# Performance work log

Hardware: AMD Instinct MI355X
Metric: run time of the kernel (lower is better)

The kernel has to match this reference:

```python
import jax, jax.numpy as jnp
import numpy as np

B, S, V = 2, 4096, 50265
L, DM, DFF = 2, 768, 3072
H, D, W = 12, 64, 256  # heads, head_dim, one-sided window (attention_window=512)
NEG = -1e9


def _ln(x, s, b, eps=1e-5):
    m = x.mean(-1, keepdims=True)
    v = ((x - m) ** 2).mean(-1, keepdims=True)
    return (x - m) * jax.lax.rsqrt(v + eps) * s + b


def _heads(y):  # [B,S,DM] -> [B,H,S,D]
    return y.reshape(B, S, H, D).transpose(0, 2, 1, 3)


def _longformer_layer(x, am, p):
    nb = S // W  # number of query blocks
    scale = 1.0 / jnp.sqrt(jnp.asarray(D, x.dtype))
    q = _heads(x @ p['Wq'] + p['bq']) * scale
    k = _heads(x @ p['Wk'] + p['bk'])
    v = _heads(x @ p['Wv'] + p['bv'])
    # overlapping key blocks: block n covers padded positions [n*W, n*W+3W)
    idx = jnp.arange(nb)[:, None] * W + jnp.arange(3 * W)[None, :]  # [nb,3W]
    kp = jnp.pad(k, ((0, 0), (0, 0), (W, W), (0, 0)))
    vp = jnp.pad(v, ((0, 0), (0, 0), (W, W), (0, 0)))
    kb = kp[:, :, idx]  # [B,H,nb,3W,D]
    vb = vp[:, :, idx]
    qb = q.reshape(B, H, nb, W, D)
    scores = jnp.einsum('bhnqd,bhnkd->bhnqk', qb, kb)  # [B,H,nb,W,3W]
    # band mask: query i attends keys within +-W
    qi = jnp.arange(W)[:, None]
    kj = jnp.arange(3 * W)[None, :]
    band = (kj >= qi) & (kj <= qi + 2 * W)  # [W,3W]
    kpos = idx - W  # global key positions, [nb,3W]
    valid = (kpos >= 0) & (kpos < S) & (kpos != 0)  # exclude global tok 0 from band
    amk = jnp.pad(am, ((0, 0), (W, W)))[:, idx] > 0  # [B,nb,3W]
    mask = band[None, None, None] & valid[None, None, :, None, :] & amk[:, None, :, None, :]
    scores = jnp.where(mask, scores, NEG).reshape(B, H, S, 3 * W)
    # global-key column: every query attends token 0 (regular K/V)
    sg = jnp.einsum('bhsd,bhd->bhs', q, k[:, :, 0])
    sg = jnp.where(am[:, None, 0:1] > 0, sg, NEG)
    attn = jax.nn.softmax(jnp.concatenate([scores, sg[..., None]], -1), axis=-1)
    a_band = attn[..., :3 * W].reshape(B, H, nb, W, 3 * W)
    out = jnp.einsum('bhnqk,bhnkd->bhnqd', a_band, vb).reshape(B, H, S, D)
    out = out + attn[..., 3 * W][..., None] * v[:, :, 0][:, :, None, :]
    # global query row (token 0): full attention with dedicated global projections
    qg = ((x[:, 0] @ p['Wqg'] + p['bqg']).reshape(B, H, D)) * scale
    kg = _heads(x @ p['Wkg'] + p['bkg'])
    vg = _heads(x @ p['Wvg'] + p['bvg'])
    sgl = jnp.einsum('bhd,bhsd->bhs', qg, kg)
    sgl = jnp.where(am[:, None, :] > 0, sgl, NEG)
    og = jnp.einsum('bhs,bhsd->bhd', jax.nn.softmax(sgl, axis=-1), vg)
    out = out.at[:, :, 0, :].set(og)
    attn_out = out.transpose(0, 2, 1, 3).reshape(B, S, DM) @ p['Wo'] + p['bo']
    x = _ln(x + attn_out, p['ln1_s'], p['ln1_b'])
    h = jax.nn.gelu(x @ p['W1'] + p['b1']) @ p['W2'] + p['b2']
    return _ln(x + h, p['ln2_s'], p['ln2_b'])


def setup_inputs() -> dict:
    key = jax.random.key(0)
    ks = iter(jax.random.split(key, 40))
    f = lambda *s: jax.random.normal(next(ks), s, jnp.float32) * 0.02
    inp = {
        'input_ids': jax.random.randint(next(ks), (B, S), 0, V),
        'attention_mask': jnp.ones((B, S), jnp.int32),
        'word_emb': f(V, DM), 'pos_emb': f(S, DM),
        'ln_e_s': jnp.ones((DM,)), 'ln_e_b': jnp.zeros((DM,)),
        'Wq': f(L, DM, DM), 'bq': jnp.zeros((L, DM)),
        'Wk': f(L, DM, DM), 'bk': jnp.zeros((L, DM)),
        'Wv': f(L, DM, DM), 'bv': jnp.zeros((L, DM)),
        'Wqg': f(L, DM, DM), 'bqg': jnp.zeros((L, DM)),
        'Wkg': f(L, DM, DM), 'bkg': jnp.zeros((L, DM)),
        'Wvg': f(L, DM, DM), 'bvg': jnp.zeros((L, DM)),
        'Wo': f(L, DM, DM), 'bo': jnp.zeros((L, DM)),
        'ln1_s': jnp.ones((L, DM)), 'ln1_b': jnp.zeros((L, DM)),
        'W1': f(L, DM, DFF), 'b1': jnp.zeros((L, DFF)),
        'W2': f(L, DFF, DM), 'b2': jnp.zeros((L, DM)),
        'ln2_s': jnp.ones((L, DM)), 'ln2_b': jnp.zeros((L, DM)),
        'Wcls': f(DM, 2), 'bcls': jnp.zeros((2,)),
    }
    return inp


def reference(input_ids, attention_mask, word_emb, pos_emb, ln_e_s, ln_e_b,
              Wq, bq, Wk, bk, Wv, bv, Wqg, bqg, Wkg, bkg, Wvg, bvg, Wo, bo,
              ln1_s, ln1_b, W1, b1, W2, b2, ln2_s, ln2_b, Wcls, bcls):
    x = word_emb[input_ids] + pos_emb[None]
    x = _ln(x, ln_e_s, ln_e_b)
    for l in range(L):
        p = dict(Wq=Wq[l], bq=bq[l], Wk=Wk[l], bk=bk[l], Wv=Wv[l], bv=bv[l],
                 Wqg=Wqg[l], bqg=bqg[l], Wkg=Wkg[l], bkg=bkg[l], Wvg=Wvg[l], bvg=bvg[l],
                 Wo=Wo[l], bo=bo[l], ln1_s=ln1_s[l], ln1_b=ln1_b[l],
                 W1=W1[l], b1=b1[l], W2=W2[l], b2=b2[l], ln2_s=ln2_s[l], ln2_b=ln2_b[l])
        x = _longformer_layer(x, attention_mask, p)
    return x[:, 0] @ Wcls + bcls  # logits [B, num_labels]
```

## Files before the change

kernel.cpp:

```cpp
#include <hip/hip_runtime.h>
#include <hip/hip_bf16.h>

#define B_   2
#define S_   4096
#define DM_  768
#define H_   12
#define D_   64
#define W_   256
#define NB_  16
#define DFF_ 3072
#define L_   2
#define QS_  3840
#define NEG_ (-1.0e9f)
#define GC_  16
#define QB_  64
#define NCH_ 18

typedef long long ll;
typedef unsigned short u16;
typedef unsigned int   u32;

typedef __attribute__((ext_vector_type(8))) short bfrag;
typedef __attribute__((ext_vector_type(4))) float ffrag;
typedef __attribute__((address_space(1))) unsigned gu32;
typedef __attribute__((address_space(3))) unsigned lu32;

__device__ __forceinline__ float b2f(u16 u){ union{u32 i; float f;} x; x.i = ((u32)u)<<16; return x.f; }
__device__ __forceinline__ u16 f2b(float f){
  __hip_bfloat16 h = __float2bfloat16(f);
  union{__hip_bfloat16 h; u16 u;} x; x.h = h; return x.u;
}
__device__ __forceinline__ void unp8(uint4 u, float* f){
  union{u32 i; float v;} a;
  a.i = u.x<<16; f[0]=a.v; a.i = u.x&0xffff0000u; f[1]=a.v;
  a.i = u.y<<16; f[2]=a.v; a.i = u.y&0xffff0000u; f[3]=a.v;
  a.i = u.z<<16; f[4]=a.v; a.i = u.z&0xffff0000u; f[5]=a.v;
  a.i = u.w<<16; f[6]=a.v; a.i = u.w&0xffff0000u; f[7]=a.v;
}
__device__ __forceinline__ void gld16(const void* g, void* l){
  __builtin_amdgcn_global_load_lds((gu32*)g, (lu32*)l, 16, 0, 0);
}
__device__ __forceinline__ float bsum256(float v, float* s4){
  #pragma unroll
  for(int o=32;o>0;o>>=1) v += __shfl_down(v,o,64);
  int w = threadIdx.x>>6;
  __syncthreads();
  if((threadIdx.x&63)==0) s4[w]=v;
  __syncthreads();
  return s4[0]+s4[1]+s4[2]+s4[3];
}
__device__ __forceinline__ float bmax256(float v, float* s4){
  #pragma unroll
  for(int o=32;o>0;o>>=1) v = fmaxf(v,__shfl_down(v,o,64));
  int w = threadIdx.x>>6;
  __syncthreads();
  if((threadIdx.x&63)==0) s4[w]=v;
  __syncthreads();
  return fmaxf(fmaxf(s4[0],s4[1]),fmaxf(s4[2],s4[3]));
}
__device__ __forceinline__ float gelu_f(float x){
  return 0.5f*x*(1.0f+tanhf(0.7978845608028654f*(x+0.044715f*x*x*x)));
}

__global__ void k_detect(const void* les, int* flag){
  unsigned u = *(const unsigned*)les;
  *flag = (u == 0x3F803F80u) ? 1 : 0;
}

__global__ void k_cvt(const void* __restrict__ src, ll soff, float* __restrict__ dst, int n, const int* flag){
  int f = *flag;
  int i = blockIdx.x*256 + threadIdx.x;
  int st = gridDim.x*256;
  if(f){
    const u16* s = (const u16*)src + soff;
    for(; i<n; i+=st) dst[i] = b2f(s[i]);
  } else {
    const float* s = (const float*)src + soff;
    for(; i<n; i+=st) dst[i] = s[i];
  }
}

struct CvtArgs { const void* src[32]; float* dst[32]; int soff[32]; int n[32]; };
__global__ void k_cvts(CvtArgs a, const int* __restrict__ flag){
  int seg = blockIdx.y;
  int i = blockIdx.x*256 + threadIdx.x;
  if(i >= a.n[seg]) return;
  int f = *flag;
  float v = f ? b2f(((const u16*)a.src[seg])[a.soff[seg]+i])
              : ((const float*)a.src[seg])[a.soff[seg]+i];
  a.dst[seg][i] = v;
}

__global__ __launch_bounds__(256) void k_tw(const void* __restrict__ src, ll soff, u16* __restrict__ dst,
    int R, int C, const int* __restrict__ flag){
  __shared__ float tile[32][33];
  int f = *flag;
  int tx = threadIdx.x & 31, ty = threadIdx.x >> 5;
  int c = blockIdx.x*32 + tx;
  #pragma unroll
  for(int i=0;i<4;i++){
    int r = blockIdx.y*32 + ty + i*8;
    float v;
    if(f) v = b2f(((const u16*)src)[soff + (ll)r*C + c]);
    else  v = ((const float*)src)[soff + (ll)r*C + c];
    tile[ty + i*8][tx] = v;
  }
  __syncthreads();
  #pragma unroll
  for(int i=0;i<4;i++){
    int orow = blockIdx.x*32 + ty + i*8;
    int oc   = blockIdx.y*32 + tx;
    dst[(ll)orow*R + oc] = f2b(tile[tx][ty + i*8]);
  }
}

struct TwArgs { const void* src[14]; ll soff[14]; u16* dst[14]; };
__global__ __launch_bounds__(256) void k_tws(TwArgs a, const int* __restrict__ flag){
  __shared__ float tile[32][33];
  int z = blockIdx.z;
  const void* src = a.src[z]; ll soff = a.soff[z]; u16* dst = a.dst[z];
  int f = *flag;
  int tx = threadIdx.x & 31, ty = threadIdx.x >> 5;
  int c = blockIdx.x*32 + tx;
  #pragma unroll
  for(int i=0;i<4;i++){
    int r = blockIdx.y*32 + ty + i*8;
    float v;
    if(f) v = b2f(((const u16*)src)[soff + (ll)r*DM_ + c]);
    else  v = ((const float*)src)[soff + (ll)r*DM_ + c];
    tile[ty + i*8][tx] = v;
  }
  __syncthreads();
  #pragma unroll
  for(int i=0;i<4;i++){
    int orow = blockIdx.x*32 + ty + i*8;
    int oc   = blockIdx.y*32 + tx;
    dst[(ll)orow*DM_ + oc] = f2b(tile[tx][ty + i*8]);
  }
}

__global__ __launch_bounds__(256) void k_embed(const int* __restrict__ ids, const void* __restrict__ wemb,
    const float* __restrict__ pos, const float* __restrict__ es, const float* __restrict__ eb,
    float* __restrict__ x, u16* __restrict__ xb, const int* flag){
  __shared__ float s4[4];
  int tok = blockIdx.x;
  int s = tok & (S_-1);
  int t = threadIdx.x;
  int id = ids[tok];
  int f = *flag;
  float v[3];
  #pragma unroll
  for(int j=0;j<3;j++){
    int i = t + j*256;
    float we = f ? b2f(((const u16*)wemb)[(ll)id*DM_ + i])
                 : ((const float*)wemb)[(ll)id*DM_ + i];
    v[j] = we + pos[s*DM_ + i];
  }
  float mean = bsum256(v[0]+v[1]+v[2], s4) * (1.0f/DM_);
  float d0=v[0]-mean, d1=v[1]-mean, d2=v[2]-mean;
  float var = bsum256(d0*d0+d1*d1+d2*d2, s4) * (1.0f/DM_);
  float r = rsqrtf(var + 1e-5f);
  #pragma unroll
  for(int j=0;j<3;j++){
    int i = t + j*256;
    float o = (v[j]-mean)*r*es[i] + eb[i];
    x[(ll)tok*DM_ + i] = o;
    xb[(ll)tok*DM_ + i] = f2b(o);
  }
}

__global__ __launch_bounds__(256) void k_rln(float* __restrict__ x, const float* __restrict__ add,
    const float* __restrict__ sc, const float* __restrict__ bi, u16* __restrict__ xb){
  __shared__ float s4[4];
  int tok = blockIdx.x;
  int t = threadIdx.x;
  float v[3];
  #pragma unroll
  for(int j=0;j<3;j++){
    int i = t + j*256;
    v[j] = x[(ll)tok*DM_+i] + add[(ll)tok*DM_+i];
  }
  float mean = bsum256(v[0]+v[1]+v[2], s4) * (1.0f/DM_);
  float d0=v[0]-mean, d1=v[1]-mean, d2=v[2]-mean;
  float var = bsum256(d0*d0+d1*d1+d2*d2, s4) * (1.0f/DM_);
  float r = rsqrtf(var + 1e-5f);
  #pragma unroll
  for(int j=0;j<3;j++){
    int i = t + j*256;
    float o = (v[j]-mean)*r*sc[i] + bi[i];
    x[(ll)tok*DM_+i] = o;
    xb[(ll)tok*DM_+i] = f2b(o);
  }
}

template<int MODE>
__global__ __launch_bounds__(256) void k_mm(const u16* __restrict__ A, const u16* __restrict__ Bt,
    const float* __restrict__ bias, void* __restrict__ Cout, int M, int N, int K){
  __shared__ __align__(16) u16 As[128*32];
  __shared__ __align__(16) u16 Bs[128*32];
  int tid = threadIdx.x, wave = tid>>6, lane = tid&63;
  int m0 = blockIdx.y*128, n0 = blockIdx.x*128;
  int wm = (wave>>1)*64, wn = (wave&1)*64;
  ffrag acc[4][4];
  #pragma unroll
  for(int i=0;i<4;i++)
    #pragma unroll
    for(int j=0;j<4;j++) acc[i][j] = (ffrag){0.f,0.f,0.f,0.f};
  int lrow = lane>>2, lseg = (lane&3)*8;
  const u16* Ap0 = A  + (ll)(m0 + wave*32 + lrow)*K + lseg;
  const u16* Bp0 = Bt + (ll)(n0 + wave*32 + lrow)*K + lseg;
  u16* AsW0 = As + (wave*2+0)*512;
  u16* AsW1 = As + (wave*2+1)*512;
  u16* BsW0 = Bs + (wave*2+0)*512;
  u16* BsW1 = Bs + (wave*2+1)*512;
  int lane15 = lane&15, quad = lane>>4;
  const u16* ArA = As + (wm + lane15)*32 + quad*8;
  const u16* BrB = Bs + (wn + lane15)*32 + quad*8;
  for(int k0=0; k0<K; k0+=32){
    __syncthreads();
    gld16(Ap0 + k0,             AsW0);
    gld16(Ap0 + k0 + (ll)16*K,  AsW1);
    gld16(Bp0 + k0,             BsW0);
    gld16(Bp0 + k0 + (ll)16*K,  BsW1);
    __syncthreads();
    bfrag af[4], bf[4];
    #pragma unroll
    for(int i=0;i<4;i++) af[i] = *(const bfrag*)(ArA + i*512);
    #pragma unroll
    for(int i=0;i<4;i++) bf[i] = *(const bfrag*)(BrB + i*512);
    #pragma unroll
    for(int i=0;i<4;i++)
      #pragma unroll
      for(int j=0;j<4;j++)
        acc[i][j] = __builtin_amdgcn_mfma_f32_16x16x32_bf16(af[i], bf[j], acc[i][j], 0, 0, 0);
  }
  #pragma unroll
  for(int mi=0;mi<4;mi++){
    #pragma unroll
    for(int ni=0;ni<4;ni++){
      int col = n0 + wn + ni*16 + lane15;
      float bv = bias[col];
      #pragma unroll
      for(int r=0;r<4;r++){
        int row = m0 + wm + mi*16 + quad*4 + r;
        float c = acc[mi][ni][r] + bv;
        if(MODE==2) c = gelu_f(c);
        if(MODE==1) ((float*)Cout)[(ll)row*N + col] = c;
        else        ((u16*)Cout)[(ll)row*N + col] = f2b(c);
      }
    }
  }
}

__global__ __launch_bounds__(256) void k_qg(const float* __restrict__ x, const u16* __restrict__ Wt,
    const float* __restrict__ bg, float* __restrict__ qg){
  int b = blockIdx.y;
  int nn = blockIdx.x*256 + threadIdx.x;
  __shared__ float xs[DM_];
  int t = threadIdx.x;
  #pragma unroll
  for(int j=0;j<3;j++) xs[t + j*256] = x[(ll)(b*S_)*DM_ + t + j*256];
  __syncthreads();
  const uint4* wr = (const uint4*)(Wt + (ll)nn*DM_);
  float acc = bg[nn];
  #pragma unroll 4
  for(int g=0; g<96; g++){
    float tf[8]; unp8(wr[g], tf);
    #pragma unroll
    for(int e=0;e<8;e++) acc = fmaf(xs[g*8+e], tf[e], acc);
  }
  qg[b*DM_ + nn] = acc;
}

__global__ __launch_bounds__(256) void k_band(const u16* __restrict__ qb, const u16* __restrict__ kb,
    const u16* __restrict__ vb, const int* __restrict__ am, u16* __restrict__ aout){
  int nq = blockIdx.x, h = blockIdx.y, b = blockIdx.z;
  int q0 = nq*QB_;
  int tid = threadIdx.x;
  int wave = tid>>6, lane = tid&63, lane15 = lane&15, quad = lane>>4;
  int wq = wave*16;
  __shared__ __align__(16) u16 Ks[32*72];
  __shared__ __align__(16) u16 Vt[64*40];
  __shared__ __align__(16) u16 Ps[4][16*40];
  __shared__ __align__(16) float cokA[QB_+2*W_];
  __shared__ __align__(16) float k0f[64];
  __shared__ __align__(16) float v0f[64];
  const int kbase = q0 - W_;
  const int am0 = am[b*S_];
  for(int i=tid; i<QB_+2*W_; i+=256){
    int kp = kbase + i;
    cokA[i] = ((kp>=1) && (kp<S_) && (am[b*S_+kp]>0)) ? 0.f : NEG_;
  }
  if(tid < 64){
    k0f[tid] = b2f(kb[(ll)(b*S_)*QS_ + h*64 + tid]);
    v0f[tid] = b2f(vb[(ll)(b*S_)*QS_ + h*64 + tid]);
  }
  bfrag aq[2];
  {
    const u16* qbase = qb + ((ll)(b*S_ + q0 + wq + lane15))*QS_ + h*64 + quad*8;
    aq[0] = *(const bfrag*)(qbase);
    aq[1] = *(const bfrag*)(qbase + 32);
  }
  ffrag ao[4];
  #pragma unroll
  for(int j=0;j<4;j++) ao[j] = (ffrag){0.f,0.f,0.f,0.f};
  float ms = -INFINITY, ls = 0.f;

  int c_lo = (kbase < 1) ? ((1 - kbase) / 32) : 0;
  if(c_lo < 0) c_lo = 0;
  int c_hi = (S_ - 1 - kbase) / 32 + 1;
  if(c_hi > NCH_) c_hi = NCH_;

  int skey = tid>>3, sseg = tid&7;
  uint4 kreg;
  union { u16 s[8]; uint4 v; } vreg;
  auto FETCH = [&](int c){
    int kp0 = kbase + c*32;
    if(kp0 >= 0 && kp0 + 31 < S_){
      kreg = *(const uint4*)(kb + ((ll)(b*S_ + kp0 + skey))*QS_ + h*64 + sseg*8);
      const u16* vp = vb + ((ll)(b*S_ + kp0 + wave*8))*QS_ + h*64 + lane;
      #pragma unroll
      for(int j=0;j<8;j++) vreg.s[j] = vp[(ll)j*QS_];
    } else {
      int kp = kp0 + skey;
      kreg = make_uint4(0,0,0,0);
      if((unsigned)kp < (unsigned)S_)
        kreg = *(const uint4*)(kb + ((ll)(b*S_+kp))*QS_ + h*64 + sseg*8);
      #pragma unroll
      for(int j=0;j<8;j++){
        int kp2 = kp0 + wave*8 + j;
        vreg.s[j] = ((unsigned)kp2 < (unsigned)S_) ? vb[((ll)(b*S_+kp2))*QS_ + h*64 + lane] : (u16)0;
      }
    }
  };
  FETCH(c_lo);

  #pragma unroll 1
  for(int c=c_lo; c<c_hi; c++){
    __syncthreads();
    *(uint4*)&Ks[skey*72 + sseg*8] = kreg;
    *(uint4*)&Vt[lane*40 + wave*8] = vreg.v;
    __syncthreads();
    if(c+1 < c_hi) FETCH(c+1);
    ffrag st0 = (ffrag){0.f,0.f,0.f,0.f};
    ffrag st1 = (ffrag){0.f,0.f,0.f,0.f};
    #pragma unroll
    for(int kc=0;kc<2;kc++){
      bfrag k0r = *(const bfrag*)&Ks[(     lane15)*72 + kc*32 + quad*8];
      bfrag k1r = *(const bfrag*)&Ks[(16 + lane15)*72 + kc*32 + quad*8];
      st0 = __builtin_amdgcn_mfma_f32_16x16x32_bf16(k0r, aq[kc], st0, 0, 0, 0);
      st1 = __builtin_amdgcn_mfma_f32_16x16x32_bf16(k1r, aq[kc], st1, 0, 0, 0);
    }
    float4 ck0 = *(const float4*)&cokA[c*32 + quad*4];
    float4 ck1 = *(const float4*)&cokA[c*32 + 16 + quad*4];
    float cka[8] = {ck0.x,ck0.y,ck0.z,ck0.w, ck1.x,ck1.y,ck1.z,ck1.w};
    int qloc = wq + lane15;
    int jg0 = c*32 + quad*4;
    float s[8];
    #pragma unroll
    for(int r=0;r<4;r++){
      s[r]   = ((unsigned)(jg0 + r      - qloc) <= 512u) ? st0[r]*0.125f + cka[r]   : NEG_;
      s[4+r] = ((unsigned)(jg0 + 16 + r - qloc) <= 512u) ? st1[r]*0.125f + cka[4+r] : NEG_;
    }
    float cm = s[0];
    #pragma unroll
    for(int r=1;r<8;r++) cm = fmaxf(cm, s[r]);
    cm = fmaxf(cm, __shfl_xor(cm,16));
    cm = fmaxf(cm, __shfl_xor(cm,32));
    float mn = fmaxf(ms, cm);
    float al = __expf(ms - mn);
    float p[8], rs = 0.f;
    #pragma unroll
    for(int r=0;r<8;r++){ p[r] = __expf(s[r] - mn); rs += p[r]; }
    rs += __shfl_xor(rs,16);
    rs += __shfl_xor(rs,32);
    ls = ls*al + rs;
    ms = mn;
    #pragma unroll
    for(int nt=0;nt<4;nt++)
      #pragma unroll
      for(int r=0;r<4;r++) ao[nt][r] *= al;
    u16 pw[8];
    #pragma unroll
    for(int r=0;r<8;r++) pw[r] = f2b(p[r]);
    uint2 w0, w1;
    w0.x = (u32)pw[0] | ((u32)pw[1]<<16); w0.y = (u32)pw[2] | ((u32)pw[3]<<16);
    w1.x = (u32)pw[4] | ((u32)pw[5]<<16); w1.y = (u32)pw[6] | ((u32)pw[7]<<16);
    *(uint2*)&Ps[wave][lane15*40 + quad*4]      = w0;
    *(uint2*)&Ps[wave][lane15*40 + 16 + quad*4] = w1;
    bfrag pf = *(const bfrag*)&Ps[wave][lane15*40 + quad*8];
    #pragma unroll
    for(int nt=0;nt<4;nt++){
      bfrag vf = *(const bfrag*)&Vt[(nt*16+lane15)*40 + quad*8];
      ao[nt] = __builtin_amdgcn_mfma_f32_16x16x32_bf16(vf, pf, ao[nt], 0, 0, 0);
    }
  }
  float sgm;
  {
    float4 ka0 = *(const float4*)&k0f[quad*8];
    float4 ka1 = *(const float4*)&k0f[quad*8 + 4];
    float4 kb0 = *(const float4*)&k0f[32 + quad*8];
    float4 kb1 = *(const float4*)&k0f[32 + quad*8 + 4];
    float k0v[16] = {ka0.x,ka0.y,ka0.z,ka0.w, ka1.x,ka1.y,ka1.z,ka1.w,
                     kb0.x,kb0.y,kb0.z,kb0.w, kb1.x,kb1.y,kb1.z,kb1.w};
    float d = 0.f;
    #pragma unroll
    for(int kc=0;kc<2;kc++)
      #pragma unroll
      for(int j=0;j<8;j++)
        d = fmaf(b2f((u16)aq[kc][j]), k0v[kc*8+j], d);
    d += __shfl_xor(d,16);
    d += __shfl_xor(d,32);
    sgm = d*0.125f + ((am0>0) ? 0.f : NEG_);
  }
  float mn = fmaxf(ms, sgm);
  float al = __expf(ms - mn);
  float pg = __expf(sgm - mn);
  float inv = 1.f / (ls*al + pg);
  u16* obase = aout + ((ll)(b*S_ + q0 + wq + lane15))*DM_ + h*64;
  #pragma unroll
  for(int nt=0;nt<4;nt++){
    float4 v0q = *(const float4*)&v0f[nt*16 + quad*4];
    float v0a[4] = {v0q.x, v0q.y, v0q.z, v0q.w};
    u16 o[4];
    #pragma unroll
    for(int r=0;r<4;r++) o[r] = f2b((ao[nt][r]*al + pg*v0a[r]) * inv);
    uint2 w;
    w.x = (u32)o[0] | ((u32)o[1]<<16);
    w.y = (u32)o[2] | ((u32)o[3]<<16);
    *(uint2*)&obase[nt*16 + quad*4] = w;
  }
}

__global__ __launch_bounds__(256) void k_gattn1(const float* __restrict__ qg, const u16* __restrict__ kg,
    const u16* __restrict__ vg, const int* __restrict__ am, float* __restrict__ part){
  int ck = blockIdx.x, h = blockIdx.y, b = blockIdx.z;
  int t = threadIdx.x;
  __shared__ float s4[4];
  __shared__ float qgs[64];
  __shared__ float ps[256];
  __shared__ float obuf[4][64];
  if(t < 64) qgs[t] = qg[b*DM_ + h*64 + t];
  __syncthreads();
  int s = ck*256 + t;
  const uint4* kr = (const uint4*)(kg + (ll)(b*S_+s)*QS_ + h*64);
  float d = 0.f;
  #pragma unroll
  for(int g=0; g<8; g++){
    float tf[8]; unp8(kr[g], tf);
    #pragma unroll
    for(int e=0;e<8;e++) d = fmaf(qgs[g*8+e], tf[e], d);
  }
  float sc = (am[b*S_+s] > 0) ? d*0.125f : NEG_;
  float m_c = bmax256(sc, s4);
  float p = __expf(sc - m_c);
  float l_c = bsum256(p, s4);
  ps[t] = p;
  __syncthreads();
  int dd = t & 63, grp = t >> 6;
  float acc = 0.f;
  const u16* vbase = vg + (ll)(b*S_ + ck*256 + grp*64)*QS_ + h*64 + dd;
  #pragma unroll 8
  for(int j=0;j<64;j++)
    acc = fmaf(ps[grp*64+j], b2f(vbase[(ll)j*QS_]), acc);
  obuf[grp][dd] = acc;
  __syncthreads();
  if(t < 64){
    float o = obuf[0][t] + obuf[1][t] + obuf[2][t] + obuf[3][t];
    float* pp = part + ((ll)(b*H_+h)*GC_ + ck)*66;
    if(t == 0){ pp[0] = m_c; pp[1] = l_c; }
    pp[2+t] = o;
  }
}

__global__ void k_gattn2(const float* __restrict__ part, u16* __restrict__ aout){
  int h = blockIdx.x, b = blockIdx.y;
  int t = threadIdx.x;
  const float* pp = part + ((ll)(b*H_+h)*GC_)*66;
  float m = -INFINITY;
  #pragma unroll
  for(int c=0;c<GC_;c++) m = fmaxf(m, pp[c*66]);
  float l = 0.f, o = 0.f;
  #pragma unroll
  for(int c=0;c<GC_;c++){
    float w = __expf(pp[c*66] - m);
    l += pp[c*66+1]*w;
    o += pp[c*66+2+t]*w;
  }
  aout[(ll)(b*S_)*DM_ + h*64 + t] = f2b(o/l);
}

__global__ __launch_bounds__(256) void k_cls(const float* __restrict__ x, const float* __restrict__ Wc,
    const float* __restrict__ bc, void* out, const int* flag){
  __shared__ float s4[4];
  int t = threadIdx.x;
  float a00=0,a01=0,a10=0,a11=0;
  for(int k=t;k<DM_;k+=256){
    float w0 = Wc[k*2], w1 = Wc[k*2+1];
    float x0 = x[k];
    float x1 = x[(ll)S_*DM_ + k];
    a00 = fmaf(x0,w0,a00); a01 = fmaf(x0,w1,a01);
    a10 = fmaf(x1,w0,a10); a11 = fmaf(x1,w1,a11);
  }
  float r00 = bsum256(a00,s4);
  float r01 = bsum256(a01,s4);
  float r10 = bsum256(a10,s4);
  float r11 = bsum256(a11,s4);
  if(t==0){
    float o[4] = {r00+bc[0], r01+bc[1], r10+bc[0], r11+bc[1]};
    if(*flag){
      __hip_bfloat16* ob = (__hip_bfloat16*)out;
      for(int i=0;i<4;i++) ob[i] = __float2bfloat16(o[i]);
    } else {
      float* of = (float*)out;
      for(int i=0;i<4;i++) of[i] = o[i];
    }
  }
}

extern "C" void kernel_launch(void* const* d_in, const int* in_sizes, int n_in,
                              void* d_out, int out_size, void* d_ws, size_t ws_size,
                              hipStream_t stream){
  char* wsb = (char*)d_ws;
  size_t off = 0;
  auto alloc = [&](size_t bytes)->size_t{ off = (off + 255) & ~(size_t)255; size_t r = off; off += bytes; return r; };
  const size_t TOK = (size_t)B_*S_;
  size_t P_flag = alloc(16);
  size_t P_pos  = alloc((size_t)S_*DM_*4);
  size_t P_les  = alloc(DM_*4), P_leb = alloc(DM_*4);
  size_t P_bqkv = alloc((size_t)L_*QS_*4);
  size_t P_bqg  = alloc((size_t)L_*DM_*4);
  size_t P_bo   = alloc((size_t)L_*DM_*4);
  size_t P_b1   = alloc((size_t)L_*DFF_*4);
  size_t P_b2   = alloc((size_t)L_*DM_*4);
  size_t P_l1s  = alloc((size_t)L_*DM_*4), P_l1b = alloc((size_t)L_*DM_*4);
  size_t P_l2s  = alloc((size_t)L_*DM_*4), P_l2b = alloc((size_t)L_*DM_*4);
  size_t P_Wc   = alloc(DM_*2*4), P_bc = alloc(64);
  size_t P_qgb  = alloc((size_t)B_*DM_*4);
  size_t P_part = alloc((size_t)B_*H_*GC_*66*4);
  size_t P_Wqkvt= alloc((size_t)L_*QS_*DM_*2);
  size_t P_Wqgt = alloc((size_t)L_*DM_*DM_*2);
  size_t P_Wot  = alloc((size_t)L_*DM_*DM_*2);
  size_t P_W1t  = alloc((size_t)L_*DM_*DFF_*2);
  size_t P_W2t  = alloc((size_t)L_*DFF_*DM_*2);
  size_t P_x    = alloc(TOK*DM_*4);
  size_t P_tmp  = alloc(TOK*DM_*4);
  size_t P_xb   = alloc(TOK*DM_*2);
  size_t P_qkv  = alloc(TOK*QS_*2);
  size_t P_aout = alloc(TOK*DM_*2);
  size_t P_h    = alloc(TOK*DFF_*2);

  int* flag = (int*)(wsb + P_flag);
  #define FP(o) ((float*)(wsb + (o)))
  #define HP(o) ((u16*)(wsb + (o)))

  k_detect<<<1,1,0,stream>>>(d_in[4], flag);

  k_cvt<<<2048,256,0,stream>>>(d_in[3], 0, FP(P_pos), S_*DM_, flag);

  {
    CvtArgs ca{};
    int ns = 0;
    auto addcv = [&](int idx, size_t dstoff, int soff, int nelem){
      ca.src[ns] = d_in[idx]; ca.dst[ns] = FP(dstoff); ca.soff[ns] = soff; ca.n[ns] = nelem; ns++;
    };
    addcv(4, P_les, 0, DM_); addcv(5, P_leb, 0, DM_);
    addcv(28, P_Wc, 0, DM_*2); addcv(29, P_bc, 0, 2);
    const int bidx[5] = {7,9,11,15,17};
    for(int l=0;l<L_;l++){
      for(int s=0;s<5;s++) addcv(bidx[s], P_bqkv + ((size_t)l*QS_ + s*DM_)*4, l*DM_, DM_);
      addcv(13, P_bqg + (size_t)l*DM_*4,  l*DM_,  DM_);
      addcv(19, P_bo  + (size_t)l*DM_*4,  l*DM_,  DM_);
      addcv(23, P_b1  + (size_t)l*DFF_*4, l*DFF_, DFF_);
      addcv(25, P_b2  + (size_t)l*DM_*4,  l*DM_,  DM_);
      addcv(20, P_l1s + (size_t)l*DM_*4,  l*DM_,  DM_);
      addcv(21, P_l1b + (size_t)l*DM_*4,  l*DM_,  DM_);
      addcv(26, P_l2s + (size_t)l*DM_*4,  l*DM_,  DM_);
      addcv(27, P_l2b + (size_t)l*DM_*4,  l*DM_,  DM_);
    }
    for(int s2=ns; s2<32; s2++){ ca.src[s2]=d_in[4]; ca.dst[s2]=FP(P_les); ca.soff[s2]=0; ca.n[s2]=0; }
    k_cvts<<<dim3(12, ns),256,0,stream>>>(ca, flag);
  }

  {
    TwArgs ta{};
    int nt_ = 0;
    const int widx[5] = {6,8,10,14,16};
    for(int l=0;l<L_;l++){
      for(int s=0;s<5;s++){
        ta.src[nt_] = d_in[widx[s]]; ta.soff[nt_] = (ll)l*DM_*DM_;
        ta.dst[nt_] = HP(P_Wqkvt) + (size_t)l*QS_*DM_ + (size_t)s*DM_*DM_; nt_++;
      }
      ta.src[nt_] = d_in[12]; ta.soff[nt_] = (ll)l*DM_*DM_;
      ta.dst[nt_] = HP(P_Wqgt) + (size_t)l*DM_*DM_; nt_++;
      ta.src[nt_] = d_in[18]; ta.soff[nt_] = (ll)l*DM_*DM_;
      ta.dst[nt_] = HP(P_Wot) + (size_t)l*DM_*DM_; nt_++;
    }
    k_tws<<<dim3(24,24,14),256,0,stream>>>(ta, flag);
  }
  for(int l=0;l<L_;l++){
    k_tw<<<dim3(DFF_/32, DM_/32),256,0,stream>>>(d_in[22], (ll)l*DM_*DFF_,
        HP(P_W1t) + (size_t)l*DFF_*DM_, DM_, DFF_, flag);
    k_tw<<<dim3(DM_/32, DFF_/32),256,0,stream>>>(d_in[24], (ll)l*DFF_*DM_,
        HP(P_W2t) + (size_t)l*DM_*DFF_, DFF_, DM_, flag);
  }

  const int* am = (const int*)d_in[1];
  k_embed<<<(int)TOK,256,0,stream>>>((const int*)d_in[0], d_in[2], FP(P_pos), FP(P_les), FP(P_leb),
                                     FP(P_x), HP(P_xb), flag);
  for(int l=0;l<L_;l++){
    const u16* Wqkvt_l = HP(P_Wqkvt) + (size_t)l*QS_*DM_;
    k_mm<0><<<dim3(QS_/128, TOK/128),256,0,stream>>>(HP(P_xb), Wqkvt_l, FP(P_bqkv) + (size_t)l*QS_,
        HP(P_qkv), (int)TOK, QS_, DM_);
    k_qg<<<dim3(3,B_),256,0,stream>>>(FP(P_x), HP(P_Wqgt) + (size_t)l*DM_*DM_, FP(P_bqg) + (size_t)l*DM_, FP(P_qgb));
    k_band<<<dim3(S_/QB_,H_,B_),256,0,stream>>>(HP(P_qkv), HP(P_qkv)+DM_, HP(P_qkv)+2*DM_, am, HP(P_aout));
    k_gattn1<<<dim3(GC_,H_,B_),256,0,stream>>>(FP(P_qgb), HP(P_qkv)+3*DM_, HP(P_qkv)+4*DM_, am, FP(P_part));
    k_gattn2<<<dim3(H_,B_),64,0,stream>>>(FP(P_part), HP(P_aout));
    k_mm<1><<<dim3(DM_/128, TOK/128),256,0,stream>>>(HP(P_aout), HP(P_Wot) + (size_t)l*DM_*DM_,
        FP(P_bo) + (size_t)l*DM_, FP(P_tmp), (int)TOK, DM_, DM_);
    k_rln<<<(int)TOK,256,0,stream>>>(FP(P_x), FP(P_tmp), FP(P_l1s) + (size_t)l*DM_, FP(P_l1b) + (size_t)l*DM_, HP(P_xb));
    k_mm<2><<<dim3(DFF_/128, TOK/128),256,0,stream>>>(HP(P_xb), HP(P_W1t) + (size_t)l*DFF_*DM_,
        FP(P_b1) + (size_t)l*DFF_, HP(P_h), (int)TOK, DFF_, DM_);
    k_mm<1><<<dim3(DM_/128, TOK/128),256,0,stream>>>(HP(P_h), HP(P_W2t) + (size_t)l*DM_*DFF_,
        FP(P_b2) + (size_t)l*DM_, FP(P_tmp), (int)TOK, DM_, DFF_);
    k_rln<<<(int)TOK,256,0,stream>>>(FP(P_x), FP(P_tmp), FP(P_l2s) + (size_t)l*DM_, FP(P_l2b) + (size_t)l*DM_, HP(P_xb));
  }
  k_cls<<<1,256,0,stream>>>(FP(P_x), FP(P_Wc), FP(P_bc), d_out, flag);
}
```

Baseline: 1.048 ms.

## Double-buffer GEMM LDS tiles and remap workgroups for XCD-aware L2 locality

The bf16 GEMM kernel now double-buffers its LDS A/B tiles, prefetching the next K-slice while MFMAs run on the current one. This cuts the loop to one barrier per iteration and overlaps global-to-LDS loads with compute. Launches switch to a 1-D grid, remapped so each group of 8 consecutive hardware-dispatched blocks (one per XCD) maps to a contiguous stripe of 8 M-tiles sharing an N-tile. This is meant to improve L2 reuse. LDS usage doubles, which may reduce occupancy.

```diff
diff --git a/kernel.cpp b/kernel.cpp
--- a/kernel.cpp
+++ b/kernel.cpp
@@ -196,10 +196,20 @@
 template<int MODE>
 __global__ __launch_bounds__(256) void k_mm(const u16* __restrict__ A, const u16* __restrict__ Bt,
     const float* __restrict__ bias, void* __restrict__ Cout, int M, int N, int K){
-  __shared__ __align__(16) u16 As[128*32];
-  __shared__ __align__(16) u16 Bs[128*32];
+  __shared__ __align__(16) u16 As[2][128*32];
+  __shared__ __align__(16) u16 Bs[2][128*32];
   int tid = threadIdx.x, wave = tid>>6, lane = tid&63;
-  int m0 = blockIdx.y*128, n0 = blockIdx.x*128;
+  int MT = M>>7, NT = N>>7;
+  int nwg = MT*NT;
+  int raw = blockIdx.x;
+  int chunk = nwg>>3;
+  int virt = ((chunk<<3)==nwg) ? ((raw&7)*chunk + (raw>>3)) : raw;
+  int per_stripe = NT<<3;
+  int sstripe = virt / per_stripe;
+  int rrem = virt - sstripe*per_stripe;
+  int nt = rrem>>3;
+  int mt = (sstripe<<3) + (rrem&7);
+  int m0 = mt<<7, n0 = nt<<7;
   int wm = (wave>>1)*64, wn = (wave&1)*64;
   ffrag acc[4][4];
   #pragma unroll
@@ -209,30 +219,41 @@
   int lrow = lane>>2, lseg = (lane&3)*8;
   const u16* Ap0 = A  + (ll)(m0 + wave*32 + lrow)*K + lseg;
   const u16* Bp0 = Bt + (ll)(n0 + wave*32 + lrow)*K + lseg;
-  u16* AsW0 = As + (wave*2+0)*512;
-  u16* AsW1 = As + (wave*2+1)*512;
-  u16* BsW0 = Bs + (wave*2+0)*512;
-  u16* BsW1 = Bs + (wave*2+1)*512;
+  u16* AsB = &As[0][0] + wave*1024;
+  u16* BsB = &Bs[0][0] + wave*1024;
   int lane15 = lane&15, quad = lane>>4;
-  const u16* ArA = As + (wm + lane15)*32 + quad*8;
-  const u16* BrB = Bs + (wn + lane15)*32 + quad*8;
-  for(int k0=0; k0<K; k0+=32){
-    __syncthreads();
-    gld16(Ap0 + k0,             AsW0);
-    gld16(Ap0 + k0 + (ll)16*K,  AsW1);
-    gld16(Bp0 + k0,             BsW0);
-    gld16(Bp0 + k0 + (ll)16*K,  BsW1);
-    __syncthreads();
+  const u16* ArA = &As[0][0] + (wm + lane15)*32 + quad*8;
+  const u16* BrB = &Bs[0][0] + (wn + lane15)*32 + quad*8;
+  int nt32 = K>>5;
+  gld16(Ap0,             AsB);
+  gld16(Ap0 + (ll)16*K,  AsB + 512);
+  gld16(Bp0,             BsB);
+  gld16(Bp0 + (ll)16*K,  BsB + 512);
+  __syncthreads();
+  int cur = 0;
+  #pragma unroll 1
+  for(int t=0; t<nt32; ++t){
+    if(t+1 < nt32){
+      int k0 = (t+1)<<5;
+      int nb = (cur^1)<<12;
+      gld16(Ap0 + k0,            AsB + nb);
+      gld16(Ap0 + k0 + (ll)16*K, AsB + nb + 512);
+      gld16(Bp0 + k0,            BsB + nb);
+      gld16(Bp0 + k0 + (ll)16*K, BsB + nb + 512);
+    }
+    int cb = cur<<12;
     bfrag af[4], bf[4];
     #pragma unroll
-    for(int i=0;i<4;i++) af[i] = *(const bfrag*)(ArA + i*512);
-    #pragma unroll
-    for(int i=0;i<4;i++) bf[i] = *(const bfrag*)(BrB + i*512);
+    for(int i=0;i<4;i++) af[i] = *(const bfrag*)(ArA + cb + i*512);
+    #pragma unroll
+    for(int i=0;i<4;i++) bf[i] = *(const bfrag*)(BrB + cb + i*512);
     #pragma unroll
     for(int i=0;i<4;i++)
       #pragma unroll
       for(int j=0;j<4;j++)
         acc[i][j] = __builtin_amdgcn_mfma_f32_16x16x32_bf16(af[i], bf[j], acc[i][j], 0, 0, 0);
+    __syncthreads();
+    cur ^= 1;
   }
   #pragma unroll
   for(int mi=0;mi<4;mi++){
@@ -608,20 +629,21 @@
   const int* am = (const int*)d_in[1];
   k_embed<<<(int)TOK,256,0,stream>>>((const int*)d_in[0], d_in[2], FP(P_pos), FP(P_les), FP(P_leb),
                                      FP(P_x), HP(P_xb), flag);
+  const int GM = (int)TOK/128;
   for(int l=0;l<L_;l++){
     const u16* Wqkvt_l = HP(P_Wqkvt) + (size_t)l*QS_*DM_;
-    k_mm<0><<<dim3(QS_/128, TOK/128),256,0,stream>>>(HP(P_xb), Wqkvt_l, FP(P_bqkv) + (size_t)l*QS_,
+    k_mm<0><<<(QS_/128)*GM,256,0,stream>>>(HP(P_xb), Wqkvt_l, FP(P_bqkv) + (size_t)l*QS_,
         HP(P_qkv), (int)TOK, QS_, DM_);
     k_qg<<<dim3(3,B_),256,0,stream>>>(FP(P_x), HP(P_Wqgt) + (size_t)l*DM_*DM_, FP(P_bqg) + (size_t)l*DM_, FP(P_qgb));
     k_band<<<dim3(S_/QB_,H_,B_),256,0,stream>>>(HP(P_qkv), HP(P_qkv)+DM_, HP(P_qkv)+2*DM_, am, HP(P_aout));
     k_gattn1<<<dim3(GC_,H_,B_),256,0,stream>>>(FP(P_qgb), HP(P_qkv)+3*DM_, HP(P_qkv)+4*DM_, am, FP(P_part));
     k_gattn2<<<dim3(H_,B_),64,0,stream>>>(FP(P_part), HP(P_aout));
-    k_mm<1><<<dim3(DM_/128, TOK/128),256,0,stream>>>(HP(P_aout), HP(P_Wot) + (size_t)l*DM_*DM_,
+    k_mm<1><<<(DM_/128)*GM,256,0,stream>>>(HP(P_aout), HP(P_Wot) + (size_t)l*DM_*DM_,
         FP(P_bo) + (size_t)l*DM_, FP(P_tmp), (int)TOK, DM_, DM_);
     k_rln<<<(int)TOK,256,0,stream>>>(FP(P_x), FP(P_tmp), FP(P_l1s) + (size_t)l*DM_, FP(P_l1b) + (size_t)l*DM_, HP(P_xb));
-    k_mm<2><<<dim3(DFF_/128, TOK/128),256,0,stream>>>(HP(P_xb), HP(P_W1t) + (size_t)l*DFF_*DM_,
+    k_mm<2><<<(DFF_/128)*GM,256,0,stream>>>(HP(P_xb), HP(P_W1t) + (size_t)l*DFF_*DM_,
         FP(P_b1) + (size_t)l*DFF_, HP(P_h), (int)TOK, DFF_, DM_);
-    k_mm<1><<<dim3(DM_/128, TOK/128),256,0,stream>>>(HP(P_h), HP(P_W2t) + (size_t)l*DM_*DFF_,
+    k_mm<1><<<(DM_/128)*GM,256,0,stream>>>(HP(P_h), HP(P_W2t) + (size_t)l*DM_*DFF_,
         FP(P_b2) + (size_t)l*DM_, FP(P_tmp), (int)TOK, DM_, DFF_);
     k_rln<<<(int)TOK,256,0,stream>>>(FP(P_x), FP(P_tmp), FP(P_l2s) + (size_t)l*DM_, FP(P_l2b) + (size_t)l*DM_, HP(P_xb));
   }
```

Measured after the change: 1.027 ms. -2.1%, faster.
